# Performance work log

Measured on AMD Instinct MI355X. Metric: run time of the kernel, lower is better.

## Reference

```python
import jax, jax.numpy as jnp
import numpy as np

N, E = 10000, 160000
IN_C, HID, OUT_C, H = 768, 256, 256, 4
EPS = 1e-5


def _gat_layer(x, src, dst, W, a_src, a_dst, b, n_nodes):
    # x: [N, Fin], W: [Fin, H*C], a_src/a_dst: [H, C], b: [C]
    h, c = a_src.shape
    xh = (x @ W).reshape(n_nodes, h, c)                      # [N,H,C]
    s = jnp.einsum('nhc,hc->nh', xh, a_src)                  # [N,H]
    d = jnp.einsum('nhc,hc->nh', xh, a_dst)                  # [N,H]
    e = jax.nn.leaky_relu(s[src] + d[dst], negative_slope=0.2)  # [E,H]
    # segment softmax over incoming edges of each dst node
    emax = jax.ops.segment_max(e, dst, num_segments=n_nodes)
    ex = jnp.exp(e - emax[dst])
    denom = jax.ops.segment_sum(ex, dst, num_segments=n_nodes)
    alpha = ex / denom[dst]                                  # [E,H]
    msg = alpha[:, :, None] * xh[src]                        # [E,H,C]
    out = jax.ops.segment_sum(msg, dst, num_segments=n_nodes)  # [N,H,C]
    return out.mean(axis=1) + b                              # concat=False: head mean


def setup_inputs() -> dict:
    key = jax.random.key(0)
    ks = jax.random.split(key, 12)
    sc1 = 1.0 / np.sqrt(IN_C)
    sc2 = 1.0 / np.sqrt(HID)
    return {
        'x': jax.random.normal(ks[0], (N, IN_C), dtype=jnp.float32),
        'edge_index': jax.random.randint(ks[1], (2, E), 0, N, dtype=jnp.int64),
        'W1': jax.random.normal(ks[2], (IN_C, H * HID), dtype=jnp.float32) * sc1,
        'att_src1': jax.random.normal(ks[3], (H, HID), dtype=jnp.float32) * sc2,
        'att_dst1': jax.random.normal(ks[4], (H, HID), dtype=jnp.float32) * sc2,
        'b1': jnp.zeros((HID,), dtype=jnp.float32),
        'gamma': jnp.ones((HID,), dtype=jnp.float32),
        'beta': jnp.zeros((HID,), dtype=jnp.float32),
        'W2': jax.random.normal(ks[5], (HID, H * OUT_C), dtype=jnp.float32) * sc2,
        'att_src2': jax.random.normal(ks[6], (H, OUT_C), dtype=jnp.float32) * sc2,
        'att_dst2': jax.random.normal(ks[7], (H, OUT_C), dtype=jnp.float32) * sc2,
        'b2': jnp.zeros((OUT_C,), dtype=jnp.float32),
    }


def reference(x, edge_index, W1, att_src1, att_dst1, b1, gamma, beta,
              W2, att_src2, att_dst2, b2):
    n = x.shape[0]
    loops = jnp.arange(n, dtype=edge_index.dtype)  # PyG GATConv adds self-loops
    src = jnp.concatenate([edge_index[0], loops])
    dst = jnp.concatenate([edge_index[1], loops])
    h = _gat_layer(x, src, dst, W1, att_src1, att_dst1, b1, n)   # [N,HID]
    # BatchNorm1d (batch statistics) + ReLU; dropout p=0 is identity
    mu = h.mean(axis=0)
    var = h.var(axis=0)
    h = (h - mu) * jax.lax.rsqrt(var + EPS) * gamma + beta
    h = jax.nn.relu(h)
    return _gat_layer(h, src, dst, W2, att_src2, att_dst2, b2, n)  # [N,OUT_C]
```

## Files before the change

### kernel.cpp

```cpp
#include <hip/hip_runtime.h>
#include <hip/hip_bf16.h>

typedef __bf16 bf16x8 __attribute__((ext_vector_type(8)));
typedef float f32x4 __attribute__((ext_vector_type(4)));
typedef unsigned short ushort8v __attribute__((ext_vector_type(8)));
typedef unsigned short ushort4v __attribute__((ext_vector_type(4)));

#define DEV __device__ __forceinline__

DEV unsigned short f2bf(float f) {
    unsigned u = __builtin_bit_cast(unsigned, f);
    unsigned r = (u + 0x7fffu + ((u >> 16) & 1u)) >> 16;
    return (unsigned short)r;
}

DEV float bf2f(unsigned short b) {
    unsigned u = ((unsigned)b) << 16;
    return __builtin_bit_cast(float, u);
}

DEV float wred_sum(float v) {
    #pragma unroll
    for (int o = 32; o > 0; o >>= 1) v += __shfl_xor(v, o, 64);
    return v;
}

__global__ __launch_bounds__(256) void prep_k(const float* __restrict__ X,
                                              unsigned short* __restrict__ XO,
                                              const float* __restrict__ W1, unsigned short* __restrict__ W1T,
                                              const float* __restrict__ W2, unsigned short* __restrict__ W2T,
                                              const int* __restrict__ ei, int* __restrict__ count,
                                              int nrows, int E, int Et,
                                              int nbA, int nbB, int nbC) {
    __shared__ unsigned short tile[32][33];
    int bid = blockIdx.x;
    int tid = threadIdx.x;
    if (bid < nbA) {
        int id = bid * 256 + tid;
        int row = id / 96;
        int k0 = (id - row * 96) * 8;
        ushort8v o;
        if (row < nrows) {
            const float* p = X + (size_t)row * 768 + k0;
            float4 a = *(const float4*)p;
            float4 b = *(const float4*)(p + 4);
            o[0] = f2bf(a.x); o[1] = f2bf(a.y); o[2] = f2bf(a.z); o[3] = f2bf(a.w);
            o[4] = f2bf(b.x); o[5] = f2bf(b.y); o[6] = f2bf(b.z); o[7] = f2bf(b.w);
        } else {
            o = (ushort8v)0;
        }
        *(ushort8v*)(XO + (size_t)id * 8) = o;
        return;
    }
    if (bid < nbA + nbB + nbC) {
        const float* W; unsigned short* WT; int K, rel;
        if (bid < nbA + nbB) { W = W1; WT = W1T; K = 768; rel = bid - nbA; }
        else                 { W = W2; WT = W2T; K = 256; rel = bid - nbA - nbB; }
        int kdim = K / 32;
        int kb = (rel % kdim) * 32, fb = (rel / kdim) * 32;
        int c = tid & 31;
        #pragma unroll
        for (int i = 0; i < 4; i++) {
            int r = (tid >> 5) + i * 8;
            tile[r][c] = f2bf(W[(size_t)(kb + r) * 1024 + fb + c]);
        }
        __syncthreads();
        #pragma unroll
        for (int i = 0; i < 4; i++) {
            int r = (tid >> 5) + i * 8;
            WT[(size_t)(fb + r) * K + kb + c] = tile[c][r];
        }
        return;
    }
    int id = (bid - nbA - nbB - nbC) * 256 + tid;
    if (id >= Et) return;
    int dst = (id < E) ? ei[E + id] : (id - E);
    atomicAdd(&count[dst], 1);
}

__global__ __launch_bounds__(256) void scanA_k(const int* __restrict__ cnt, int* __restrict__ loc,
                                               int* __restrict__ bsum, int n) {
    __shared__ int ws[4];
    int b = blockIdx.x, tid = threadIdx.x, wave = tid >> 6, lane = tid & 63;
    int gi = b * 256 + tid;
    int v = (gi < n) ? cnt[gi] : 0;
    int s = v;
    #pragma unroll
    for (int o = 1; o < 64; o <<= 1) { int t = __shfl_up(s, o, 64); if (lane >= o) s += t; }
    if (lane == 63) ws[wave] = s;
    __syncthreads();
    int add = 0;
    #pragma unroll
    for (int w = 0; w < 3; w++) if (wave > w) add += ws[w];
    int excl = s - v + add;
    if (gi < n) loc[gi] = excl;
    if (tid == 255) bsum[b] = excl + v;
}

__global__ void scanB_k(int* __restrict__ bsum, int nb) {
    int lane = threadIdx.x;
    int v = (lane < nb) ? bsum[lane] : 0;
    int s = v;
    #pragma unroll
    for (int o = 1; o < 64; o <<= 1) { int t = __shfl_up(s, o, 64); if (lane >= o) s += t; }
    if (lane < nb) bsum[lane] = s - v;
}

__global__ __launch_bounds__(256) void scanC_k(int* __restrict__ indptr, int* __restrict__ cursor,
                                               const int* __restrict__ bsum, int n, int Et) {
    int b = blockIdx.x, gi = b * 256 + threadIdx.x;
    if (gi < n) {
        int v = indptr[gi] + bsum[b];
        indptr[gi] = v;
        cursor[gi] = v;
    }
    if (gi == 0) indptr[n] = Et;
}

__global__ __launch_bounds__(256) void scatter_k(const int* __restrict__ ei, int* __restrict__ cursor,
                                                 int* __restrict__ srcs, int E, int Et) {
    int id = blockIdx.x * 256 + threadIdx.x;
    if (id >= Et) return;
    int s, d;
    if (id < E) { s = ei[id]; d = ei[E + id]; } else { s = id - E; d = s; }
    int pos = atomicAdd(&cursor[d], 1);
    srcs[pos] = s;
}

__global__ __launch_bounds__(256) void gemm_k(const unsigned short* __restrict__ A,
                                              const unsigned short* __restrict__ B,
                                              unsigned short* __restrict__ C, int K) {
    __shared__ unsigned short lds_a[128 * 64];
    __shared__ unsigned short lds_b[128 * 64];
    int m0 = blockIdx.x * 128, n0 = blockIdx.y * 128;
    int tid = threadIdx.x, wave = tid >> 6, lane = tid & 63;
    int wr = wave >> 1, wc = wave & 1;
    f32x4 acc[4][4] = {};
    int slotbase = wave * 256;
    for (int kt = 0; kt < K; kt += 64) {
        #pragma unroll
        for (int t = 0; t < 4; t++) {
            int slot = slotbase + t * 64 + lane;
            int row = slot >> 3;
            int cp = slot & 7;
            int cc = cp ^ (row & 7);
            const unsigned short* ga = A + (size_t)(m0 + row) * K + kt + cc * 8;
            const unsigned short* gb = B + (size_t)(n0 + row) * K + kt + cc * 8;
            __builtin_amdgcn_global_load_lds((const __attribute__((address_space(1))) void*)ga,
                (__attribute__((address_space(3))) void*)(lds_a + (size_t)(slotbase + t * 64) * 8), 16, 0, 0);
            __builtin_amdgcn_global_load_lds((const __attribute__((address_space(1))) void*)gb,
                (__attribute__((address_space(3))) void*)(lds_b + (size_t)(slotbase + t * 64) * 8), 16, 0, 0);
        }
        __syncthreads();
        #pragma unroll
        for (int kk = 0; kk < 2; kk++) {
            bf16x8 af[4], bg[4];
            #pragma unroll
            for (int m = 0; m < 4; m++) {
                int row = wr * 64 + m * 16 + (lane & 15);
                int c = kk * 4 + (lane >> 4);
                int cp = c ^ (row & 7);
                af[m] = *(const bf16x8*)(lds_a + (row * 8 + cp) * 8);
            }
            #pragma unroll
            for (int nn = 0; nn < 4; nn++) {
                int row = wc * 64 + nn * 16 + (lane & 15);
                int c = kk * 4 + (lane >> 4);
                int cp = c ^ (row & 7);
                bg[nn] = *(const bf16x8*)(lds_b + (row * 8 + cp) * 8);
            }
            #pragma unroll
            for (int m = 0; m < 4; m++)
                #pragma unroll
                for (int nn = 0; nn < 4; nn++)
                    acc[m][nn] = __builtin_amdgcn_mfma_f32_16x16x32_bf16(af[m], bg[nn], acc[m][nn], 0, 0, 0);
        }
        __syncthreads();
    }
    #pragma unroll
    for (int m = 0; m < 4; m++) {
        #pragma unroll
        for (int nn = 0; nn < 4; nn++) {
            int c = n0 + wc * 64 + nn * 16 + (lane & 15);
            #pragma unroll
            for (int j = 0; j < 4; j++) {
                int r = m0 + wr * 64 + m * 16 + (lane >> 4) * 4 + j;
                C[(size_t)r * 1024 + c] = f2bf(acc[m][nn][j]);
            }
        }
    }
}

__global__ __launch_bounds__(256) void sd_k(const unsigned short* __restrict__ xh,
                                            const float* __restrict__ asrc, const float* __restrict__ adst,
                                            float* __restrict__ s, float* __restrict__ d) {
    int n = blockIdx.x;
    int tid = threadIdx.x, h = tid >> 6, lane = tid & 63;
    ushort4v u = *(const ushort4v*)(xh + (size_t)n * 1024 + h * 256 + lane * 4);
    float4 va = *(const float4*)(asrc + h * 256 + lane * 4);
    float4 vd = *(const float4*)(adst + h * 256 + lane * 4);
    float x0 = bf2f(u[0]), x1 = bf2f(u[1]), x2 = bf2f(u[2]), x3 = bf2f(u[3]);
    float ps = x0 * va.x + x1 * va.y + x2 * va.z + x3 * va.w;
    float pd = x0 * vd.x + x1 * vd.y + x2 * vd.z + x3 * vd.w;
    ps = wred_sum(ps);
    pd = wred_sum(pd);
    if (lane == 0) { s[n * 4 + h] = ps; d[n * 4 + h] = pd; }
}

__global__ __launch_bounds__(256) void aggr_k(const unsigned short* __restrict__ xh,
                                              const float* __restrict__ svec, const float* __restrict__ dvec,
                                              const int* __restrict__ indptr, const int* __restrict__ srcs,
                                              const float* __restrict__ bias, float* __restrict__ out) {
    __shared__ float ob[2][16][64];
    __shared__ float lpart[2][4];
    __shared__ int   stab[4][64];
    __shared__ float wtab[4][64][4];
    int tid = threadIdx.x, wave = tid >> 6, lane = tid & 63;
    int nid = wave >> 1, parity = wave & 1;
    int n = blockIdx.x * 2 + nid;
    int head = lane >> 4;
    int start = indptr[n], end = indptr[n + 1];
    int cnt = end - start;
    float4 dv4 = ((const float4*)dvec)[n];
    const ushort8v* xb = (const ushort8v*)xh;
    size_t loff = (size_t)(lane << 1);
    float acc[16];
    #pragma unroll
    for (int j = 0; j < 16; j++) acc[j] = 0.f;
    float ls0 = 0.f, ls1 = 0.f, ls2 = 0.f, ls3 = 0.f;
    int nw = (cnt > parity) ? ((cnt - parity + 1) >> 1) : 0;
    for (int c0 = 0; c0 < nw; c0 += 64) {
        int m = min(64, nw - c0);
        if (lane < m) {
            int j = c0 + lane;
            int sv = srcs[start + parity + 2 * j];
            float4 s4 = ((const float4*)svec)[sv];
            float e0 = s4.x + dv4.x, e1 = s4.y + dv4.y, e2 = s4.z + dv4.z, e3 = s4.w + dv4.w;
            e0 = e0 > 0.f ? e0 : 0.2f * e0; e1 = e1 > 0.f ? e1 : 0.2f * e1;
            e2 = e2 > 0.f ? e2 : 0.2f * e2; e3 = e3 > 0.f ? e3 : 0.2f * e3;
            float w0 = __expf(e0), w1 = __expf(e1), w2 = __expf(e2), w3 = __expf(e3);
            ls0 += w0; ls1 += w1; ls2 += w2; ls3 += w3;
            stab[wave][lane] = sv;
            float4 wv = {w0, w1, w2, w3};
            *(float4*)&wtab[wave][lane][0] = wv;
        }
        int k = 0;
        for (; k + 4 <= m; k += 4) {
            int s0 = stab[wave][k], s1 = stab[wave][k + 1];
            int s2 = stab[wave][k + 2], s3 = stab[wave][k + 3];
            float w0 = wtab[wave][k][head],     w1 = wtab[wave][k + 1][head];
            float w2 = wtab[wave][k + 2][head], w3 = wtab[wave][k + 3][head];
            ushort8v a0 = xb[(size_t)s0 * 128 + loff], a1 = xb[(size_t)s0 * 128 + loff + 1];
            ushort8v b0 = xb[(size_t)s1 * 128 + loff], b1 = xb[(size_t)s1 * 128 + loff + 1];
            ushort8v c0v = xb[(size_t)s2 * 128 + loff], c1v = xb[(size_t)s2 * 128 + loff + 1];
            ushort8v d0 = xb[(size_t)s3 * 128 + loff], d1 = xb[(size_t)s3 * 128 + loff + 1];
            #pragma unroll
            for (int j = 0; j < 8; j++) {
                acc[j]     += w0 * bf2f(a0[j]) + w1 * bf2f(b0[j]) + w2 * bf2f(c0v[j]) + w3 * bf2f(d0[j]);
                acc[8 + j] += w0 * bf2f(a1[j]) + w1 * bf2f(b1[j]) + w2 * bf2f(c1v[j]) + w3 * bf2f(d1[j]);
            }
        }
        for (; k < m; k++) {
            int s0 = stab[wave][k];
            float w0 = wtab[wave][k][head];
            ushort8v a0 = xb[(size_t)s0 * 128 + loff], a1 = xb[(size_t)s0 * 128 + loff + 1];
            #pragma unroll
            for (int j = 0; j < 8; j++) {
                acc[j]     += w0 * bf2f(a0[j]);
                acc[8 + j] += w0 * bf2f(a1[j]);
            }
        }
    }
    ls0 = wred_sum(ls0); ls1 = wred_sum(ls1); ls2 = wred_sum(ls2); ls3 = wred_sum(ls3);
    if (parity == 1) {
        #pragma unroll
        for (int j = 0; j < 16; j++) ob[nid][j][lane] = acc[j];
        if (lane == 0) {
            lpart[nid][0] = ls0; lpart[nid][1] = ls1;
            lpart[nid][2] = ls2; lpart[nid][3] = ls3;
        }
    }
    __syncthreads();
    if (parity == 0) {
        #pragma unroll
        for (int j = 0; j < 16; j++) acc[j] += ob[nid][j][lane];
        float Lown = head < 2 ? (head == 0 ? ls0 : ls1) : (head == 2 ? ls2 : ls3);
        float L = Lown + lpart[nid][head];
        float inv = 0.25f / L;
        #pragma unroll
        for (int j = 0; j < 16; j++) {
            float r = acc[j] * inv;
            r += __shfl_xor(r, 16, 64);
            r += __shfl_xor(r, 32, 64);
            acc[j] = r;
        }
        if (lane < 16) {
            int c0 = lane << 4;
            const float4* bp = (const float4*)(bias + c0);
            float* op = out + (size_t)n * 256 + c0;
            #pragma unroll
            for (int q = 0; q < 4; q++) {
                float4 bv = bp[q];
                float4 ov;
                ov.x = acc[q * 4 + 0] + bv.x;
                ov.y = acc[q * 4 + 1] + bv.y;
                ov.z = acc[q * 4 + 2] + bv.z;
                ov.w = acc[q * 4 + 3] + bv.w;
                *(float4*)(op + q * 4) = ov;
            }
        }
    }
}

__global__ __launch_bounds__(256) void bnstat_k(const float* __restrict__ h, float* __restrict__ bnsum,
                                                float* __restrict__ bnss, int n, int rpb) {
    int c = threadIdx.x;
    int r0 = blockIdx.x * rpb;
    int r1 = min(r0 + rpb, n);
    float s = 0.f, q = 0.f;
    for (int r = r0; r < r1; r++) {
        float v = h[(size_t)r * 256 + c];
        s += v; q += v * v;
    }
    atomicAdd(&bnsum[c], s);
    atomicAdd(&bnss[c], q);
}

__global__ __launch_bounds__(256) void bnapply_k(const float* __restrict__ h, const float* __restrict__ bnsum,
                                                 const float* __restrict__ bnss, const float* __restrict__ gamma,
                                                 const float* __restrict__ beta, unsigned short* __restrict__ o,
                                                 int nrows, float invn) {
    int row = blockIdx.x, c = threadIdx.x;
    unsigned short r;
    if (row < nrows) {
        float mu = bnsum[c] * invn;
        float var = bnss[c] * invn - mu * mu;
        float v = (h[(size_t)row * 256 + c] - mu) * rsqrtf(var + 1e-5f) * gamma[c] + beta[c];
        v = fmaxf(v, 0.f);
        r = f2bf(v);
    } else {
        r = 0;
    }
    o[(size_t)row * 256 + c] = r;
}

extern "C" void kernel_launch(void* const* d_in, const int* in_sizes, int n_in,
                              void* d_out, int out_size, void* d_ws, size_t ws_size,
                              hipStream_t stream) {
    const float* x     = (const float*)d_in[0];
    const int*   ei    = (const int*)d_in[1];
    const float* W1    = (const float*)d_in[2];
    const float* as1   = (const float*)d_in[3];
    const float* ad1   = (const float*)d_in[4];
    const float* b1    = (const float*)d_in[5];
    const float* gamma = (const float*)d_in[6];
    const float* beta  = (const float*)d_in[7];
    const float* W2    = (const float*)d_in[8];
    const float* as2   = (const float*)d_in[9];
    const float* ad2   = (const float*)d_in[10];
    const float* b2    = (const float*)d_in[11];
    float* out = (float*)d_out;

    const int N = in_sizes[0] / 768;
    const int E = in_sizes[1] / 2;
    const int Et = E + N;
    const int Mpad = ((N + 127) / 128) * 128;

    char* w = (char*)d_ws;
    size_t o = 0;
    auto alloc = [&](size_t b) { size_t r = o; o += (b + 255) & ~(size_t)255; return r; };
    unsigned short* xh     = (unsigned short*)(w + alloc((size_t)Mpad * 1024 * 2));
    unsigned short* xbf    = (unsigned short*)(w + alloc((size_t)Mpad * 768 * 2));
    unsigned short* hbf    = (unsigned short*)(w + alloc((size_t)Mpad * 256 * 2));
    unsigned short* w1t    = (unsigned short*)(w + alloc((size_t)1024 * 768 * 2));
    unsigned short* w2t    = (unsigned short*)(w + alloc((size_t)1024 * 256 * 2));
    float*          svec   = (float*)(w + alloc((size_t)N * 4 * 4));
    float*          dvec   = (float*)(w + alloc((size_t)N * 4 * 4));
    float*          hbuf   = (float*)(w + alloc((size_t)N * 256 * 4));
    int*            indptr = (int*)(w + alloc((size_t)(N + 1) * 4));
    int*            cursor = (int*)(w + alloc((size_t)N * 4));
    int*            count  = (int*)(w + alloc((size_t)N * 4));
    int*            bsum   = (int*)(w + alloc(256));
    float*          bnsum  = (float*)(w + alloc(256 * 4));
    float*          bnss   = (float*)(w + alloc(256 * 4));
    int*            srcs   = (int*)(w + alloc((size_t)Et * 4));

    hipMemsetAsync(count, 0, (size_t)N * 4, stream);
    hipMemsetAsync(bnsum, 0, 2048, stream);

    int nbA = (Mpad * 96) / 256;
    int nbB = (768 / 32) * (1024 / 32);
    int nbC = (256 / 32) * (1024 / 32);
    int nbD = (Et + 255) / 256;
    prep_k<<<nbA + nbB + nbC + nbD, 256, 0, stream>>>(x, xbf, W1, w1t, W2, w2t, ei, count,
                                                      N, E, Et, nbA, nbB, nbC);
    int nbS = (N + 255) / 256;
    scanA_k<<<nbS, 256, 0, stream>>>(count, indptr, bsum, N);
    scanB_k<<<1, 64, 0, stream>>>(bsum, nbS);
    scanC_k<<<nbS, 256, 0, stream>>>(indptr, cursor, bsum, N, Et);
    scatter_k<<<(Et + 255) / 256, 256, 0, stream>>>(ei, cursor, srcs, E, Et);

    gemm_k<<<dim3(Mpad / 128, 8), 256, 0, stream>>>(xbf, w1t, xh, 768);
    sd_k<<<N, 256, 0, stream>>>(xh, as1, ad1, svec, dvec);
    aggr_k<<<N / 2, 256, 0, stream>>>(xh, svec, dvec, indptr, srcs, b1, hbuf);

    bnstat_k<<<80, 256, 0, stream>>>(hbuf, bnsum, bnss, N, (N + 79) / 80);
    bnapply_k<<<Mpad, 256, 0, stream>>>(hbuf, bnsum, bnss, gamma, beta, hbf, N, 1.0f / (float)N);

    gemm_k<<<dim3(Mpad / 128, 8), 256, 0, stream>>>(hbf, w2t, xh, 256);
    sd_k<<<N, 256, 0, stream>>>(xh, as2, ad2, svec, dvec);
    aggr_k<<<N / 2, 256, 0, stream>>>(xh, svec, dvec, indptr, srcs, b2, out);
}
```

Measured before the change: 307.9 us.

## Restructure GAT aggregation to loop over heads with per-lane channel accumulation

The aggregation kernel now loops over the four heads, so each lane accumulates 4 channels of one head instead of 16 channels spread across heads. This removes the cross-lane shuffle reduction over heads and cuts accumulator registers. The cost is that edge weights and source indices are recomputed and reloaded per head, with an extra block barrier per head. The gather loop is unrolled to 8 edges of 8-byte loads, trading wider per-lane loads for more loads in flight.

```diff
diff --git a/kernel.cpp b/kernel.cpp
--- a/kernel.cpp
+++ b/kernel.cpp
@@ -211,104 +211,94 @@
                                               const float* __restrict__ svec, const float* __restrict__ dvec,
                                               const int* __restrict__ indptr, const int* __restrict__ srcs,
                                               const float* __restrict__ bias, float* __restrict__ out) {
-    __shared__ float ob[2][16][64];
-    __shared__ float lpart[2][4];
     __shared__ int   stab[4][64];
-    __shared__ float wtab[4][64][4];
+    __shared__ float wtab[4][64];
+    __shared__ float lpart[4][2][2];
+    __shared__ float ob[2][4][64];
     int tid = threadIdx.x, wave = tid >> 6, lane = tid & 63;
     int nid = wave >> 1, parity = wave & 1;
     int n = blockIdx.x * 2 + nid;
-    int head = lane >> 4;
     int start = indptr[n], end = indptr[n + 1];
     int cnt = end - start;
+    int nw = (cnt > parity) ? ((cnt - parity + 1) >> 1) : 0;
     float4 dv4 = ((const float4*)dvec)[n];
-    const ushort8v* xb = (const ushort8v*)xh;
-    size_t loff = (size_t)(lane << 1);
-    float acc[16];
-    #pragma unroll
-    for (int j = 0; j < 16; j++) acc[j] = 0.f;
-    float ls0 = 0.f, ls1 = 0.f, ls2 = 0.f, ls3 = 0.f;
-    int nw = (cnt > parity) ? ((cnt - parity + 1) >> 1) : 0;
-    for (int c0 = 0; c0 < nw; c0 += 64) {
-        int m = min(64, nw - c0);
-        if (lane < m) {
-            int j = c0 + lane;
-            int sv = srcs[start + parity + 2 * j];
-            float4 s4 = ((const float4*)svec)[sv];
-            float e0 = s4.x + dv4.x, e1 = s4.y + dv4.y, e2 = s4.z + dv4.z, e3 = s4.w + dv4.w;
-            e0 = e0 > 0.f ? e0 : 0.2f * e0; e1 = e1 > 0.f ? e1 : 0.2f * e1;
-            e2 = e2 > 0.f ? e2 : 0.2f * e2; e3 = e3 > 0.f ? e3 : 0.2f * e3;
-            float w0 = __expf(e0), w1 = __expf(e1), w2 = __expf(e2), w3 = __expf(e3);
-            ls0 += w0; ls1 += w1; ls2 += w2; ls3 += w3;
-            stab[wave][lane] = sv;
-            float4 wv = {w0, w1, w2, w3};
-            *(float4*)&wtab[wave][lane][0] = wv;
-        }
-        int k = 0;
-        for (; k + 4 <= m; k += 4) {
-            int s0 = stab[wave][k], s1 = stab[wave][k + 1];
-            int s2 = stab[wave][k + 2], s3 = stab[wave][k + 3];
-            float w0 = wtab[wave][k][head],     w1 = wtab[wave][k + 1][head];
-            float w2 = wtab[wave][k + 2][head], w3 = wtab[wave][k + 3][head];
-            ushort8v a0 = xb[(size_t)s0 * 128 + loff], a1 = xb[(size_t)s0 * 128 + loff + 1];
-            ushort8v b0 = xb[(size_t)s1 * 128 + loff], b1 = xb[(size_t)s1 * 128 + loff + 1];
-            ushort8v c0v = xb[(size_t)s2 * 128 + loff], c1v = xb[(size_t)s2 * 128 + loff + 1];
-            ushort8v d0 = xb[(size_t)s3 * 128 + loff], d1 = xb[(size_t)s3 * 128 + loff + 1];
-            #pragma unroll
-            for (int j = 0; j < 8; j++) {
-                acc[j]     += w0 * bf2f(a0[j]) + w1 * bf2f(b0[j]) + w2 * bf2f(c0v[j]) + w3 * bf2f(d0[j]);
-                acc[8 + j] += w0 * bf2f(a1[j]) + w1 * bf2f(b1[j]) + w2 * bf2f(c1v[j]) + w3 * bf2f(d1[j]);
-            }
-        }
-        for (; k < m; k++) {
-            int s0 = stab[wave][k];
-            float w0 = wtab[wave][k][head];
-            ushort8v a0 = xb[(size_t)s0 * 128 + loff], a1 = xb[(size_t)s0 * 128 + loff + 1];
-            #pragma unroll
-            for (int j = 0; j < 8; j++) {
-                acc[j]     += w0 * bf2f(a0[j]);
-                acc[8 + j] += w0 * bf2f(a1[j]);
-            }
-        }
-    }
-    ls0 = wred_sum(ls0); ls1 = wred_sum(ls1); ls2 = wred_sum(ls2); ls3 = wred_sum(ls3);
+    float dhv[4] = {dv4.x, dv4.y, dv4.z, dv4.w};
+    const ushort4v* xb4 = (const ushort4v*)xh;
+    float acc[4] = {0.f, 0.f, 0.f, 0.f};
+    #pragma unroll
+    for (int h = 0; h < 4; h++) {
+        float dh = dhv[h];
+        float phacc[4] = {0.f, 0.f, 0.f, 0.f};
+        float ls = 0.f;
+        for (int c0 = 0; c0 < nw; c0 += 64) {
+            int m = min(64, nw - c0);
+            if (lane < m) {
+                int j = c0 + lane;
+                int sv = srcs[start + parity + 2 * j];
+                float e = svec[sv * 4 + h] + dh;
+                e = e > 0.f ? e : 0.2f * e;
+                float wgt = __expf(e);
+                ls += wgt;
+                stab[wave][lane] = sv;
+                wtab[wave][lane] = wgt;
+            }
+            size_t hoff = (size_t)(h * 64 + lane);
+            int k = 0;
+            for (; k + 8 <= m; k += 8) {
+                int s0 = stab[wave][k],     s1 = stab[wave][k + 1];
+                int s2 = stab[wave][k + 2], s3 = stab[wave][k + 3];
+                int s4 = stab[wave][k + 4], s5 = stab[wave][k + 5];
+                int s6 = stab[wave][k + 6], s7 = stab[wave][k + 7];
+                float w0 = wtab[wave][k],     w1 = wtab[wave][k + 1];
+                float w2 = wtab[wave][k + 2], w3 = wtab[wave][k + 3];
+                float w4 = wtab[wave][k + 4], w5 = wtab[wave][k + 5];
+                float w6 = wtab[wave][k + 6], w7 = wtab[wave][k + 7];
+                ushort4v a0 = xb4[(size_t)s0 * 256 + hoff];
+                ushort4v a1 = xb4[(size_t)s1 * 256 + hoff];
+                ushort4v a2 = xb4[(size_t)s2 * 256 + hoff];
+                ushort4v a3 = xb4[(size_t)s3 * 256 + hoff];
+                ushort4v a4 = xb4[(size_t)s4 * 256 + hoff];
+                ushort4v a5 = xb4[(size_t)s5 * 256 + hoff];
+                ushort4v a6 = xb4[(size_t)s6 * 256 + hoff];
+                ushort4v a7 = xb4[(size_t)s7 * 256 + hoff];
+                #pragma unroll
+                for (int j = 0; j < 4; j++) {
+                    phacc[j] += w0 * bf2f(a0[j]) + w1 * bf2f(a1[j])
+                              + w2 * bf2f(a2[j]) + w3 * bf2f(a3[j])
+                              + w4 * bf2f(a4[j]) + w5 * bf2f(a5[j])
+                              + w6 * bf2f(a6[j]) + w7 * bf2f(a7[j]);
+                }
+            }
+            for (; k < m; k++) {
+                int s0 = stab[wave][k];
+                float w0 = wtab[wave][k];
+                ushort4v a0 = xb4[(size_t)s0 * 256 + hoff];
+                #pragma unroll
+                for (int j = 0; j < 4; j++) phacc[j] += w0 * bf2f(a0[j]);
+            }
+        }
+        ls = wred_sum(ls);
+        if (lane == 0) lpart[h][nid][parity] = ls;
+        __syncthreads();
+        float L = lpart[h][nid][0] + lpart[h][nid][1];
+        float sc = 0.25f / L;
+        #pragma unroll
+        for (int j = 0; j < 4; j++) acc[j] += sc * phacc[j];
+    }
     if (parity == 1) {
         #pragma unroll
-        for (int j = 0; j < 16; j++) ob[nid][j][lane] = acc[j];
-        if (lane == 0) {
-            lpart[nid][0] = ls0; lpart[nid][1] = ls1;
-            lpart[nid][2] = ls2; lpart[nid][3] = ls3;
-        }
+        for (int j = 0; j < 4; j++) ob[nid][j][lane] = acc[j];
     }
     __syncthreads();
     if (parity == 0) {
         #pragma unroll
-        for (int j = 0; j < 16; j++) acc[j] += ob[nid][j][lane];
-        float Lown = head < 2 ? (head == 0 ? ls0 : ls1) : (head == 2 ? ls2 : ls3);
-        float L = Lown + lpart[nid][head];
-        float inv = 0.25f / L;
-        #pragma unroll
-        for (int j = 0; j < 16; j++) {
-            float r = acc[j] * inv;
-            r += __shfl_xor(r, 16, 64);
-            r += __shfl_xor(r, 32, 64);
-            acc[j] = r;
-        }
-        if (lane < 16) {
-            int c0 = lane << 4;
-            const float4* bp = (const float4*)(bias + c0);
-            float* op = out + (size_t)n * 256 + c0;
-            #pragma unroll
-            for (int q = 0; q < 4; q++) {
-                float4 bv = bp[q];
-                float4 ov;
-                ov.x = acc[q * 4 + 0] + bv.x;
-                ov.y = acc[q * 4 + 1] + bv.y;
-                ov.z = acc[q * 4 + 2] + bv.z;
-                ov.w = acc[q * 4 + 3] + bv.w;
-                *(float4*)(op + q * 4) = ov;
-            }
-        }
+        for (int j = 0; j < 4; j++) acc[j] += ob[nid][j][lane];
+        int c0 = lane * 4;
+        float4 bv = *(const float4*)(bias + c0);
+        float4 ov;
+        ov.x = acc[0] + bv.x; ov.y = acc[1] + bv.y;
+        ov.z = acc[2] + bv.z; ov.w = acc[3] + bv.w;
+        *(float4*)(out + (size_t)n * 256 + c0) = ov;
     }
 }
 
```

Measured after the change: 364.7 us. 1.18x slower.

## Fuse attention score dot products into GEMM epilogue and merge scan kernels

Applied to the files above, without the earlier changes.

The per-node attention projections (s, d) are now computed in the GEMM epilogue from the fp32 accumulators, reduced across 16 lanes and accumulated with atomics into zeroed s/d buffers. This removes the separate sd_k launch and its reread of xh. The block-sum scan kernel is also folded into scanC_k, where each block sums the preceding block totals itself. The cost is extra memsets, atomic traffic and epilogue work in the GEMM. Scores now come from unrounded fp32 accumulators rather than the bf16 values, which slightly changes numerics.

```diff
diff --git a/kernel.cpp b/kernel.cpp
--- a/kernel.cpp
+++ b/kernel.cpp
@@ -97,20 +97,22 @@
     if (tid == 255) bsum[b] = excl + v;
 }
 
-__global__ void scanB_k(int* __restrict__ bsum, int nb) {
-    int lane = threadIdx.x;
-    int v = (lane < nb) ? bsum[lane] : 0;
-    int s = v;
-    #pragma unroll
-    for (int o = 1; o < 64; o <<= 1) { int t = __shfl_up(s, o, 64); if (lane >= o) s += t; }
-    if (lane < nb) bsum[lane] = s - v;
-}
-
 __global__ __launch_bounds__(256) void scanC_k(int* __restrict__ indptr, int* __restrict__ cursor,
-                                               const int* __restrict__ bsum, int n, int Et) {
-    int b = blockIdx.x, gi = b * 256 + threadIdx.x;
+                                               const int* __restrict__ bsum, int n, int Et, int nb) {
+    __shared__ int boff_s;
+    int b = blockIdx.x, tid = threadIdx.x;
+    if (tid < 64) {
+        int lane = tid;
+        int v = (lane < nb && lane < b) ? bsum[lane] : 0;
+        #pragma unroll
+        for (int o = 32; o > 0; o >>= 1) v += __shfl_xor(v, o, 64);
+        if (lane == 0) boff_s = v;
+    }
+    __syncthreads();
+    int boff = boff_s;
+    int gi = b * 256 + tid;
     if (gi < n) {
-        int v = indptr[gi] + bsum[b];
+        int v = indptr[gi] + boff;
         indptr[gi] = v;
         cursor[gi] = v;
     }
@@ -129,7 +131,11 @@
 
 __global__ __launch_bounds__(256) void gemm_k(const unsigned short* __restrict__ A,
                                               const unsigned short* __restrict__ B,
-                                              unsigned short* __restrict__ C, int K) {
+                                              unsigned short* __restrict__ C, int K,
+                                              const float* __restrict__ asrc,
+                                              const float* __restrict__ adst,
+                                              float* __restrict__ sv, float* __restrict__ dv,
+                                              int nN) {
     __shared__ unsigned short lds_a[128 * 64];
     __shared__ unsigned short lds_b[128 * 64];
     int m0 = blockIdx.x * 128, n0 = blockIdx.y * 128;
@@ -189,22 +195,38 @@
             }
         }
     }
-}
-
-__global__ __launch_bounds__(256) void sd_k(const unsigned short* __restrict__ xh,
-                                            const float* __restrict__ asrc, const float* __restrict__ adst,
-                                            float* __restrict__ s, float* __restrict__ d) {
-    int n = blockIdx.x;
-    int tid = threadIdx.x, h = tid >> 6, lane = tid & 63;
-    ushort4v u = *(const ushort4v*)(xh + (size_t)n * 1024 + h * 256 + lane * 4);
-    float4 va = *(const float4*)(asrc + h * 256 + lane * 4);
-    float4 vd = *(const float4*)(adst + h * 256 + lane * 4);
-    float x0 = bf2f(u[0]), x1 = bf2f(u[1]), x2 = bf2f(u[2]), x3 = bf2f(u[3]);
-    float ps = x0 * va.x + x1 * va.y + x2 * va.z + x3 * va.w;
-    float pd = x0 * vd.x + x1 * vd.y + x2 * vd.z + x3 * vd.w;
-    ps = wred_sum(ps);
-    pd = wred_sum(pd);
-    if (lane == 0) { s[n * 4 + h] = ps; d[n * 4 + h] = pd; }
+    int headc = n0 >> 8;
+    float asv[4], adv[4];
+    #pragma unroll
+    for (int nn = 0; nn < 4; nn++) {
+        int c = n0 + wc * 64 + nn * 16 + (lane & 15);
+        asv[nn] = asrc[c];
+        adv[nn] = adst[c];
+    }
+    #pragma unroll
+    for (int m = 0; m < 4; m++) {
+        #pragma unroll
+        for (int j = 0; j < 4; j++) {
+            float ps = 0.f, pd = 0.f;
+            #pragma unroll
+            for (int nn = 0; nn < 4; nn++) {
+                ps += acc[m][nn][j] * asv[nn];
+                pd += acc[m][nn][j] * adv[nn];
+            }
+            #pragma unroll
+            for (int o2 = 1; o2 < 16; o2 <<= 1) {
+                ps += __shfl_xor(ps, o2, 64);
+                pd += __shfl_xor(pd, o2, 64);
+            }
+            if ((lane & 15) == 0) {
+                int r = m0 + wr * 64 + m * 16 + (lane >> 4) * 4 + j;
+                if (r < nN) {
+                    atomicAdd(&sv[r * 4 + headc], ps);
+                    atomicAdd(&dv[r * 4 + headc], pd);
+                }
+            }
+        }
+    }
 }
 
 __global__ __launch_bounds__(256) void aggr_k(const unsigned short* __restrict__ xh,
@@ -374,8 +396,11 @@
     unsigned short* hbf    = (unsigned short*)(w + alloc((size_t)Mpad * 256 * 2));
     unsigned short* w1t    = (unsigned short*)(w + alloc((size_t)1024 * 768 * 2));
     unsigned short* w2t    = (unsigned short*)(w + alloc((size_t)1024 * 256 * 2));
-    float*          svec   = (float*)(w + alloc((size_t)N * 4 * 4));
-    float*          dvec   = (float*)(w + alloc((size_t)N * 4 * 4));
+    size_t svoff = alloc((size_t)N * 4 * 4);
+    float*          svec   = (float*)(w + svoff);
+    size_t dvoff = alloc((size_t)N * 4 * 4);
+    float*          dvec   = (float*)(w + dvoff);
+    size_t sdbytes = dvoff + (size_t)N * 16 - svoff;
     float*          hbuf   = (float*)(w + alloc((size_t)N * 256 * 4));
     int*            indptr = (int*)(w + alloc((size_t)(N + 1) * 4));
     int*            cursor = (int*)(w + alloc((size_t)N * 4));
@@ -387,6 +412,7 @@
 
     hipMemsetAsync(count, 0, (size_t)N * 4, stream);
     hipMemsetAsync(bnsum, 0, 2048, stream);
+    hipMemsetAsync(svec, 0, sdbytes, stream);
 
     int nbA = (Mpad * 96) / 256;
     int nbB = (768 / 32) * (1024 / 32);
@@ -396,18 +422,16 @@
                                                       N, E, Et, nbA, nbB, nbC);
     int nbS = (N + 255) / 256;
     scanA_k<<<nbS, 256, 0, stream>>>(count, indptr, bsum, N);
-    scanB_k<<<1, 64, 0, stream>>>(bsum, nbS);
-    scanC_k<<<nbS, 256, 0, stream>>>(indptr, cursor, bsum, N, Et);
+    scanC_k<<<nbS, 256, 0, stream>>>(indptr, cursor, bsum, N, Et, nbS);
     scatter_k<<<(Et + 255) / 256, 256, 0, stream>>>(ei, cursor, srcs, E, Et);
 
-    gemm_k<<<dim3(Mpad / 128, 8), 256, 0, stream>>>(xbf, w1t, xh, 768);
-    sd_k<<<N, 256, 0, stream>>>(xh, as1, ad1, svec, dvec);
+    gemm_k<<<dim3(Mpad / 128, 8), 256, 0, stream>>>(xbf, w1t, xh, 768, as1, ad1, svec, dvec, N);
     aggr_k<<<N / 2, 256, 0, stream>>>(xh, svec, dvec, indptr, srcs, b1, hbuf);
 
     bnstat_k<<<80, 256, 0, stream>>>(hbuf, bnsum, bnss, N, (N + 79) / 80);
     bnapply_k<<<Mpad, 256, 0, stream>>>(hbuf, bnsum, bnss, gamma, beta, hbf, N, 1.0f / (float)N);
 
-    gemm_k<<<dim3(Mpad / 128, 8), 256, 0, stream>>>(hbf, w2t, xh, 256);
-    sd_k<<<N, 256, 0, stream>>>(xh, as2, ad2, svec, dvec);
+    hipMemsetAsync(svec, 0, sdbytes, stream);
+    gemm_k<<<dim3(Mpad / 128, 8), 256, 0, stream>>>(hbf, w2t, xh, 256, as2, ad2, svec, dvec, N);
     aggr_k<<<N / 2, 256, 0, stream>>>(xh, svec, dvec, indptr, srcs, b2, out);
 }
```

Result: slower. 339.7 us (+10.3%).
